# Optimization experiments

Hardware: AMD Instinct MI355X
Metric: run time of the kernel (lower is better)

## Reference

```python
import jax, jax.numpy as jnp
import numpy as np

IN_DIM = 256
LATENT = 1024
OUT_DIM = 256
B = 128
T = 1024


def setup_inputs() -> dict:
    key = jax.random.key(0)
    k1, k2, k3, k4 = jax.random.split(key, 4)
    # torch Linear weight layout: [out_features, in_features]
    bound_lin = 1.0 / np.sqrt(IN_DIM + LATENT)
    bound_dec = 1.0 / np.sqrt(LATENT)
    return {
        "x": jax.random.normal(k1, (B, T, IN_DIM), dtype=jnp.float32),
        "W_lin": jax.random.uniform(k2, (LATENT, IN_DIM + LATENT), minval=-bound_lin, maxval=bound_lin, dtype=jnp.float32),
        "W_dec": jax.random.uniform(k3, (OUT_DIM, LATENT), minval=-bound_dec, maxval=bound_dec, dtype=jnp.float32),
        "b_dec": jax.random.uniform(k4, (OUT_DIM,), minval=-bound_dec, maxval=bound_dec, dtype=jnp.float32),
    }


def reference(x, W_lin, W_dec, b_dec):
    # cat((x_t, h), dim=1) @ W_lin.T == x_t @ Wx.T + h @ Wh.T
    Wx = W_lin[:, :IN_DIM]      # [latent, in_dim]
    Wh = W_lin[:, IN_DIM:]      # [latent, latent]
    h0 = jnp.zeros((x.shape[0], LATENT), dtype=x.dtype)

    def step(h, x_t):
        h_new = jnp.tanh(x_t @ Wx.T + h @ Wh.T)
        return h_new, None

    # scan over time: x -> [T, B, in_dim]
    h_final, _ = jax.lax.scan(step, h0, jnp.swapaxes(x, 0, 1))
    return jnp.tanh(h_final @ W_dec.T + b_dec)
```

## Files before the change

### kernel.cpp

```cpp
#include <hip/hip_runtime.h>
#include <hip/hip_bf16.h>
#include <stdint.h>

#define B_    128
#define T_    1024
#define IN_   256
#define L_    1024
#define OUT_  256
#define KTOT  1280

#define GROUPS 8
#define WPG    32
#define NB     16
#define NC     32
#define PAD_K  1288
#define LDS_W_BYTES (NC * PAD_K * 2)
#define RED_BYTES   (8 * 4 * 64 * 4)
#define STILE_BYTES (16 * 32 * 2)
#define LDS_TOTAL   (LDS_W_BYTES + RED_BYTES + STILE_BYTES)

using short8 = __attribute__((ext_vector_type(8))) short;
using bf16x8 = __attribute__((ext_vector_type(8))) __bf16;
using f32x4  = __attribute__((ext_vector_type(4))) float;

__device__ __forceinline__ unsigned short f2b(float f) {
  unsigned u = __builtin_bit_cast(unsigned, f);
  u += 0x7FFFu + ((u >> 16) & 1u);
  return (unsigned short)(u >> 16);
}
__device__ __forceinline__ float b2f(unsigned short h) {
  unsigned u = ((unsigned)h) << 16;
  return __builtin_bit_cast(float, u);
}
__device__ __forceinline__ float fast_tanh(float z) {
  z = fminf(fmaxf(z, -30.f), 30.f);
  float e2 = __expf(2.f * z);
  return __fdividef(e2 - 1.f, e2 + 1.f);
}

__global__ __launch_bounds__(256, 1)
void rnn_persistent(const float* __restrict__ x, const float* __restrict__ Wlin,
                    unsigned short* __restrict__ h0buf, unsigned short* __restrict__ h1buf,
                    unsigned int* __restrict__ flags)
{
  extern __shared__ char smem[];
  short* Wlds = (short*)smem;
  float* red  = (float*)(smem + LDS_W_BYTES);
  unsigned short* stile = (unsigned short*)(smem + LDS_W_BYTES + RED_BYTES);

  const int tid = threadIdx.x;
  const int g   = blockIdx.x & 7;
  const int w   = blockIdx.x >> 3;
  const int bb  = g * NB;
  const int cc  = w * NC;
  unsigned int* myflag = flags + (size_t)(g * WPG + w) * 16;

  for (int r = 0; r < NC; ++r) {
    const float* wrow = Wlin + (size_t)(cc + r) * KTOT;
    for (int k = tid; k < KTOT; k += 256)
      Wlds[r * PAD_K + k] = (short)f2b(wrow[k]);
  }
  __syncthreads();

  const int wv   = tid >> 6;
  const int l    = tid & 63;
  const int lrow = l & 15;
  const int lk   = (l >> 4) * 8;

  for (int t = 0; t < T_; ++t) {
    const unsigned short* hcur = (t & 1) ? h1buf : h0buf;
    unsigned short*       hnxt = (t & 1) ? h0buf : h1buf;

    f32x4 acc0 = {0.f, 0.f, 0.f, 0.f};
    f32x4 acc1 = {0.f, 0.f, 0.f, 0.f};

    #pragma unroll
    for (int j = 0; j < 2; ++j) {
      const int kk    = wv + 4 * j;
      const int kbase = kk * 32 + lk;
      const float* xp = x + ((size_t)(bb + lrow) * T_ + t) * IN_ + kbase;
      f32x4 x0 = *(const f32x4*)xp;
      f32x4 x1 = *(const f32x4*)(xp + 4);
      short8 a;
      a[0] = (short)f2b(x0[0]); a[1] = (short)f2b(x0[1]);
      a[2] = (short)f2b(x0[2]); a[3] = (short)f2b(x0[3]);
      a[4] = (short)f2b(x1[0]); a[5] = (short)f2b(x1[1]);
      a[6] = (short)f2b(x1[2]); a[7] = (short)f2b(x1[3]);
      short8 b0 = *(const short8*)&Wlds[lrow        * PAD_K + kbase];
      short8 b1 = *(const short8*)&Wlds[(lrow + 16) * PAD_K + kbase];
      acc0 = __builtin_amdgcn_mfma_f32_16x16x32_bf16(
               __builtin_bit_cast(bf16x8, a), __builtin_bit_cast(bf16x8, b0), acc0, 0, 0, 0);
      acc1 = __builtin_amdgcn_mfma_f32_16x16x32_bf16(
               __builtin_bit_cast(bf16x8, a), __builtin_bit_cast(bf16x8, b1), acc1, 0, 0, 0);
    }

    if (t > 0) {
      if (wv == 0) {
        unsigned int* fp = flags + (size_t)(g * WPG + (l & 31)) * 16;
        while (true) {
          unsigned int v = __hip_atomic_load(fp, __ATOMIC_RELAXED, __HIP_MEMORY_SCOPE_AGENT);
          if (__all((int)(v >= (unsigned)t))) break;
          __builtin_amdgcn_s_sleep(1);
        }
      }
      __syncthreads();

      short8 hf[8];
      #pragma unroll
      for (int j = 2; j < 10; ++j) {
        const int kk    = wv + 4 * j;
        const int kbase = kk * 32 + lk - IN_;
        const unsigned short* p = hcur + (size_t)(bb + lrow) * L_ + kbase;
        asm volatile("global_load_dwordx4 %0, %1, off sc0 sc1"
                     : "=v"(hf[j - 2]) : "v"(p) : "memory");
      }
      asm volatile("s_waitcnt vmcnt(0)" ::: "memory");
      __builtin_amdgcn_sched_barrier(0);

      #pragma unroll
      for (int j = 2; j < 10; ++j) {
        const int kbase = (wv + 4 * j) * 32 + lk;
        short8 b0 = *(const short8*)&Wlds[lrow        * PAD_K + kbase];
        short8 b1 = *(const short8*)&Wlds[(lrow + 16) * PAD_K + kbase];
        acc0 = __builtin_amdgcn_mfma_f32_16x16x32_bf16(
                 __builtin_bit_cast(bf16x8, hf[j - 2]), __builtin_bit_cast(bf16x8, b0), acc0, 0, 0, 0);
        acc1 = __builtin_amdgcn_mfma_f32_16x16x32_bf16(
                 __builtin_bit_cast(bf16x8, hf[j - 2]), __builtin_bit_cast(bf16x8, b1), acc1, 0, 0, 0);
      }
    }

    #pragma unroll
    for (int j = 0; j < 4; ++j) {
      red[((wv * 2 + 0) * 4 + j) * 64 + l] = acc0[j];
      red[((wv * 2 + 1) * 4 + j) * 64 + l] = acc1[j];
    }
    __syncthreads();
    if (wv < 2) {
      const int tile = wv;
      #pragma unroll
      for (int j = 0; j < 4; ++j) {
        float s = red[((0 * 2 + tile) * 4 + j) * 64 + l]
                + red[((1 * 2 + tile) * 4 + j) * 64 + l]
                + red[((2 * 2 + tile) * 4 + j) * 64 + l]
                + red[((3 * 2 + tile) * 4 + j) * 64 + l];
        float hv = fast_tanh(s);
        const int row = (l >> 4) * 4 + j;
        const int col = tile * 16 + (l & 15);
        stile[row * 32 + col] = f2b(hv);
      }
    }
    __syncthreads();

    {
      const int row  = tid >> 4;
      const int dcol = tid & 15;
      unsigned int v = ((const unsigned int*)stile)[tid];
      unsigned int* dp = (unsigned int*)(hnxt + (size_t)(bb + row) * L_ + cc) + dcol;
      asm volatile("global_store_dword %0, %1, off sc0 sc1" :: "v"(dp), "v"(v) : "memory");
    }
    asm volatile("s_waitcnt vmcnt(0)" ::: "memory");
    __syncthreads();
    if (tid == 0)
      __hip_atomic_store(myflag, (unsigned)(t + 1), __ATOMIC_RELAXED, __HIP_MEMORY_SCOPE_AGENT);
  }
}

__global__ __launch_bounds__(256)
void decode_kernel(const unsigned short* __restrict__ hfin,
                   const float* __restrict__ Wdec, const float* __restrict__ bdec,
                   float* __restrict__ out)
{
  __shared__ float hrow[L_];
  const int b = blockIdx.x, tid = threadIdx.x;
  for (int k = tid; k < L_; k += 256)
    hrow[k] = b2f(hfin[b * L_ + k]);
  __syncthreads();
  float s = bdec[tid];
  const float* wr = Wdec + (size_t)tid * L_;
  #pragma unroll 4
  for (int k = 0; k < L_; k += 4) {
    f32x4 wq = *(const f32x4*)(wr + k);
    s += hrow[k] * wq[0] + hrow[k+1] * wq[1] + hrow[k+2] * wq[2] + hrow[k+3] * wq[3];
  }
  out[b * OUT_ + tid] = fast_tanh(s);
}

extern "C" void kernel_launch(void* const* d_in, const int* in_sizes, int n_in,
                              void* d_out, int out_size, void* d_ws, size_t ws_size,
                              hipStream_t stream)
{
  const float* x    = (const float*)d_in[0];
  const float* Wlin = (const float*)d_in[1];
  const float* Wdec = (const float*)d_in[2];
  const float* bdec = (const float*)d_in[3];
  float* out = (float*)d_out;

  unsigned short* h0 = (unsigned short*)d_ws;
  unsigned short* h1 = h0 + (size_t)B_ * L_;
  unsigned int* flags = (unsigned int*)((char*)d_ws + (size_t)2 * B_ * L_ * 2);

  hipMemsetAsync(flags, 0, (size_t)GROUPS * WPG * 16 * sizeof(unsigned int), stream);

  hipFuncSetAttribute((const void*)rnn_persistent,
                      hipFuncAttributeMaxDynamicSharedMemorySize, LDS_TOTAL);

  hipLaunchKernelGGL(rnn_persistent, dim3(GROUPS * WPG), dim3(256), LDS_TOTAL, stream,
                     x, Wlin, h0, h1, flags);
  hipLaunchKernelGGL(decode_kernel, dim3(B_), dim3(256), 0, stream,
                     h0, Wdec, bdec, out);
}
```

Measured before the change: 3.290 ms.

## Replace per-step flag barrier with sentinel-tagged 4-slot hidden-state ring

Drops the per-block progress flags and the spin on them. Hidden states now go into a 4-slot ring whose entries are reset to a NaN sentinel two steps ahead. Readers load h directly and reload any chunk still holding the sentinel, so data arrival itself acts as the sync and one __syncthreads plus the flag store are removed each step. A retry cap stops the spin after a fixed count and then goes ahead with possibly stale data, and correctness depends on store ordering across slots.

```diff
diff --git a/kernel.cpp b/kernel.cpp
--- a/kernel.cpp
+++ b/kernel.cpp
@@ -19,9 +19,14 @@
 #define STILE_BYTES (16 * 32 * 2)
 #define LDS_TOTAL   (LDS_W_BYTES + RED_BYTES + STILE_BYTES)
 
+#define SENT      0x7F807F80u
+#define SLOT      (B_ * L_)
+#define RETRY_CAP 20000
+
 using short8 = __attribute__((ext_vector_type(8))) short;
 using bf16x8 = __attribute__((ext_vector_type(8))) __bf16;
 using f32x4  = __attribute__((ext_vector_type(4))) float;
+using u32x4  = __attribute__((ext_vector_type(4))) unsigned;
 
 __device__ __forceinline__ unsigned short f2b(float f) {
   unsigned u = __builtin_bit_cast(unsigned, f);
@@ -37,11 +42,26 @@
   float e2 = __expf(2.f * z);
   return __fdividef(e2 - 1.f, e2 + 1.f);
 }
+__device__ __forceinline__ int chunk_ok(short8 c) {
+  u32x4 u = __builtin_bit_cast(u32x4, c);
+  return (u[0] != SENT) & (u[1] != SENT) & (u[2] != SENT) & (u[3] != SENT);
+}
+__device__ __forceinline__ void st_dw(unsigned int* p, unsigned int v) {
+  asm volatile("global_store_dword %0, %1, off sc0 sc1" :: "v"(p), "v"(v) : "memory");
+}
+__device__ __forceinline__ void ld_x4(short8& d, const unsigned short* p) {
+  asm volatile("global_load_dwordx4 %0, %1, off sc0 sc1" : "=v"(d) : "v"(p) : "memory");
+}
+
+__global__ void init_ws(unsigned int* ring_dw) {
+  size_t i = (size_t)blockIdx.x * 256 + threadIdx.x;
+  const size_t total = (size_t)4 * SLOT / 2;
+  for (size_t k = i; k < total; k += (size_t)256 * 256) ring_dw[k] = SENT;
+}
 
 __global__ __launch_bounds__(256, 1)
 void rnn_persistent(const float* __restrict__ x, const float* __restrict__ Wlin,
-                    unsigned short* __restrict__ h0buf, unsigned short* __restrict__ h1buf,
-                    unsigned int* __restrict__ flags)
+                    unsigned short* __restrict__ ring)
 {
   extern __shared__ char smem[];
   short* Wlds = (short*)smem;
@@ -53,7 +73,6 @@
   const int w   = blockIdx.x >> 3;
   const int bb  = g * NB;
   const int cc  = w * NC;
-  unsigned int* myflag = flags + (size_t)(g * WPG + w) * 16;
 
   for (int r = 0; r < NC; ++r) {
     const float* wrow = Wlin + (size_t)(cc + r) * KTOT;
@@ -66,10 +85,26 @@
   const int l    = tid & 63;
   const int lrow = l & 15;
   const int lk   = (l >> 4) * 8;
+  const int prow = tid >> 4;
+  const int pcol = tid & 15;
 
   for (int t = 0; t < T_; ++t) {
-    const unsigned short* hcur = (t & 1) ? h1buf : h0buf;
-    unsigned short*       hnxt = (t & 1) ? h0buf : h1buf;
+    unsigned short* hcur = ring + (size_t)(t & 3) * SLOT;
+    unsigned short* hnxt = ring + (size_t)((t + 1) & 3) * SLOT;
+
+    {
+      unsigned int* rp = (unsigned int*)(ring + (size_t)((t + 2) & 3) * SLOT
+                                         + (size_t)(bb + prow) * L_ + cc) + pcol;
+      st_dw(rp, SENT);
+    }
+
+    short8 hf[8];
+    const unsigned short* hbase = hcur + (size_t)(bb + lrow) * L_ + wv * 32 + lk;
+    if (t > 0) {
+      #pragma unroll
+      for (int j = 0; j < 8; ++j)
+        ld_x4(hf[j], hbase + j * 128);
+    }
 
     f32x4 acc0 = {0.f, 0.f, 0.f, 0.f};
     f32x4 acc1 = {0.f, 0.f, 0.f, 0.f};
@@ -95,37 +130,33 @@
     }
 
     if (t > 0) {
-      if (wv == 0) {
-        unsigned int* fp = flags + (size_t)(g * WPG + (l & 31)) * 16;
-        while (true) {
-          unsigned int v = __hip_atomic_load(fp, __ATOMIC_RELAXED, __HIP_MEMORY_SCOPE_AGENT);
-          if (__all((int)(v >= (unsigned)t))) break;
-          __builtin_amdgcn_s_sleep(1);
-        }
-      }
-      __syncthreads();
-
-      short8 hf[8];
-      #pragma unroll
-      for (int j = 2; j < 10; ++j) {
-        const int kk    = wv + 4 * j;
-        const int kbase = kk * 32 + lk - IN_;
-        const unsigned short* p = hcur + (size_t)(bb + lrow) * L_ + kbase;
-        asm volatile("global_load_dwordx4 %0, %1, off sc0 sc1"
-                     : "=v"(hf[j - 2]) : "v"(p) : "memory");
-      }
       asm volatile("s_waitcnt vmcnt(0)" ::: "memory");
       __builtin_amdgcn_sched_barrier(0);
 
+      bool okj[8] = {false, false, false, false, false, false, false, false};
+      int remaining = 8, tries = 0;
+      while (true) {
+        #pragma unroll
+        for (int j = 0; j < 8; ++j)
+          if (!okj[j] && __all(chunk_ok(hf[j]))) { okj[j] = true; --remaining; }
+        if (remaining == 0) break;
+        if (++tries > RETRY_CAP) break;
+        #pragma unroll
+        for (int j = 0; j < 8; ++j)
+          if (!okj[j]) ld_x4(hf[j], hbase + j * 128);
+        asm volatile("s_waitcnt vmcnt(0)" ::: "memory");
+        __builtin_amdgcn_sched_barrier(0);
+      }
+
       #pragma unroll
-      for (int j = 2; j < 10; ++j) {
-        const int kbase = (wv + 4 * j) * 32 + lk;
+      for (int j = 0; j < 8; ++j) {
+        const int kbase = IN_ + wv * 32 + j * 128 + lk;
         short8 b0 = *(const short8*)&Wlds[lrow        * PAD_K + kbase];
         short8 b1 = *(const short8*)&Wlds[(lrow + 16) * PAD_K + kbase];
         acc0 = __builtin_amdgcn_mfma_f32_16x16x32_bf16(
-                 __builtin_bit_cast(bf16x8, hf[j - 2]), __builtin_bit_cast(bf16x8, b0), acc0, 0, 0, 0);
+                 __builtin_bit_cast(bf16x8, hf[j]), __builtin_bit_cast(bf16x8, b0), acc0, 0, 0, 0);
         acc1 = __builtin_amdgcn_mfma_f32_16x16x32_bf16(
-                 __builtin_bit_cast(bf16x8, hf[j - 2]), __builtin_bit_cast(bf16x8, b1), acc1, 0, 0, 0);
+                 __builtin_bit_cast(bf16x8, hf[j]), __builtin_bit_cast(bf16x8, b1), acc1, 0, 0, 0);
       }
     }
 
@@ -144,24 +175,17 @@
                 + red[((2 * 2 + tile) * 4 + j) * 64 + l]
                 + red[((3 * 2 + tile) * 4 + j) * 64 + l];
         float hv = fast_tanh(s);
-        const int row = (l >> 4) * 4 + j;
-        const int col = tile * 16 + (l & 15);
-        stile[row * 32 + col] = f2b(hv);
+        stile[((l >> 4) * 4 + j) * 32 + tile * 16 + (l & 15)] = f2b(hv);
       }
     }
     __syncthreads();
 
+    asm volatile("s_waitcnt vmcnt(0)" ::: "memory");
     {
-      const int row  = tid >> 4;
-      const int dcol = tid & 15;
       unsigned int v = ((const unsigned int*)stile)[tid];
-      unsigned int* dp = (unsigned int*)(hnxt + (size_t)(bb + row) * L_ + cc) + dcol;
-      asm volatile("global_store_dword %0, %1, off sc0 sc1" :: "v"(dp), "v"(v) : "memory");
-    }
-    asm volatile("s_waitcnt vmcnt(0)" ::: "memory");
-    __syncthreads();
-    if (tid == 0)
-      __hip_atomic_store(myflag, (unsigned)(t + 1), __ATOMIC_RELAXED, __HIP_MEMORY_SCOPE_AGENT);
+      unsigned int* dp = (unsigned int*)(hnxt + (size_t)(bb + prow) * L_ + cc) + pcol;
+      st_dw(dp, v);
+    }
   }
 }
 
@@ -195,17 +219,15 @@
   const float* bdec = (const float*)d_in[3];
   float* out = (float*)d_out;
 
-  unsigned short* h0 = (unsigned short*)d_ws;
-  unsigned short* h1 = h0 + (size_t)B_ * L_;
-  unsigned int* flags = (unsigned int*)((char*)d_ws + (size_t)2 * B_ * L_ * 2);
-
-  hipMemsetAsync(flags, 0, (size_t)GROUPS * WPG * 16 * sizeof(unsigned int), stream);
+  unsigned short* ring = (unsigned short*)d_ws;
 
   hipFuncSetAttribute((const void*)rnn_persistent,
                       hipFuncAttributeMaxDynamicSharedMemorySize, LDS_TOTAL);
 
+  hipLaunchKernelGGL(init_ws, dim3(256), dim3(256), 0, stream,
+                     (unsigned int*)ring);
   hipLaunchKernelGGL(rnn_persistent, dim3(GROUPS * WPG), dim3(256), LDS_TOTAL, stream,
-                     x, Wlin, h0, h1, flags);
+                     x, Wlin, ring);
   hipLaunchKernelGGL(decode_kernel, dim3(B_), dim3(256), 0, stream,
-                     h0, Wdec, bdec, out);
-}
+                     ring, Wdec, bdec, out);
+}
```

Measured after the change: 4.521 ms. 37.4% more time.

## Halve workgroups per batch group and consume hidden-state slices as producers signal

Applied to the files above, without the earlier changes.

The partition changes from 32 to 16 workgroups per batch group, so each workgroup computes 64 latent columns. The input-projection weights now live in registers, and LDS holds only the recurrent weights. The global barrier, where one wave waited on all 32 flags, is replaced by per-wave polling of just the 4 producer flags that wave depends on. Each wave then loads and multiplies hidden-state slices as soon as they are ready, so compute overlaps with waiting and a block-wide sync goes away. The output staging tile is dropped in favour of direct 16-bit stores. This trades half as many CUs doing twice the MFMA work per step for fewer flags to poll and finer-grained overlap.

```diff
diff --git a/kernel.cpp b/kernel.cpp
--- a/kernel.cpp
+++ b/kernel.cpp
@@ -10,14 +10,13 @@
 #define KTOT  1280
 
 #define GROUPS 8
-#define WPG    32
+#define WPG    16
 #define NB     16
-#define NC     32
-#define PAD_K  1288
-#define LDS_W_BYTES (NC * PAD_K * 2)
-#define RED_BYTES   (8 * 4 * 64 * 4)
-#define STILE_BYTES (16 * 32 * 2)
-#define LDS_TOTAL   (LDS_W_BYTES + RED_BYTES + STILE_BYTES)
+#define NC     64
+#define PADW   1032
+#define LDS_W_BYTES (NC * PADW * 2)
+#define RED_BYTES   (4 * 4 * 4 * 64 * 4)
+#define LDS_TOTAL   (LDS_W_BYTES + RED_BYTES)
 
 using short8 = __attribute__((ext_vector_type(8))) short;
 using bf16x8 = __attribute__((ext_vector_type(8))) __bf16;
@@ -36,6 +35,20 @@
   z = fminf(fmaxf(z, -30.f), 30.f);
   float e2 = __expf(2.f * z);
   return __fdividef(e2 - 1.f, e2 + 1.f);
+}
+__device__ __forceinline__ void st_us(unsigned short* p, unsigned short v) {
+  asm volatile("global_store_short %0, %1, off sc0 sc1" :: "v"(p), "v"(v) : "memory");
+}
+__device__ __forceinline__ void ld_x4(short8& d, const unsigned short* p) {
+  asm volatile("global_load_dwordx4 %0, %1, off sc0 sc1" : "=v"(d) : "v"(p) : "memory");
+}
+__device__ __forceinline__ short8 cvt8(f32x4 a, f32x4 b) {
+  short8 v;
+  v[0] = (short)f2b(a[0]); v[1] = (short)f2b(a[1]);
+  v[2] = (short)f2b(a[2]); v[3] = (short)f2b(a[3]);
+  v[4] = (short)f2b(b[0]); v[5] = (short)f2b(b[1]);
+  v[6] = (short)f2b(b[2]); v[7] = (short)f2b(b[3]);
+  return v;
 }
 
 __global__ __launch_bounds__(256, 1)
@@ -46,118 +59,112 @@
   extern __shared__ char smem[];
   short* Wlds = (short*)smem;
   float* red  = (float*)(smem + LDS_W_BYTES);
-  unsigned short* stile = (unsigned short*)(smem + LDS_W_BYTES + RED_BYTES);
 
   const int tid = threadIdx.x;
   const int g   = blockIdx.x & 7;
   const int w   = blockIdx.x >> 3;
   const int bb  = g * NB;
   const int cc  = w * NC;
+
+  for (int r = 0; r < NC; ++r) {
+    const float* wrow = Wlin + (size_t)(cc + r) * KTOT + IN_;
+    for (int k = tid; k < L_; k += 256)
+      Wlds[r * PADW + k] = (short)f2b(wrow[k]);
+  }
+
+  const int wv  = tid >> 6;
+  const int l   = tid & 63;
+  const int lr  = l & 15;
+  const int lk8 = (l >> 4) * 8;
+
+  short8 wx[4][2];
+  #pragma unroll
+  for (int nt = 0; nt < 4; ++nt) {
+    #pragma unroll
+    for (int ks = 0; ks < 2; ++ks) {
+      const float* wp = Wlin + (size_t)(cc + nt * 16 + lr) * KTOT + wv * 64 + ks * 32 + lk8;
+      wx[nt][ks] = cvt8(*(const f32x4*)wp, *(const f32x4*)(wp + 4));
+    }
+  }
+  __syncthreads();
+
   unsigned int* myflag = flags + (size_t)(g * WPG + w) * 16;
-
-  for (int r = 0; r < NC; ++r) {
-    const float* wrow = Wlin + (size_t)(cc + r) * KTOT;
-    for (int k = tid; k < KTOT; k += 256)
-      Wlds[r * PAD_K + k] = (short)f2b(wrow[k]);
-  }
-  __syncthreads();
-
-  const int wv   = tid >> 6;
-  const int l    = tid & 63;
-  const int lrow = l & 15;
-  const int lk   = (l >> 4) * 8;
 
   for (int t = 0; t < T_; ++t) {
     const unsigned short* hcur = (t & 1) ? h1buf : h0buf;
     unsigned short*       hnxt = (t & 1) ? h0buf : h1buf;
 
-    f32x4 acc0 = {0.f, 0.f, 0.f, 0.f};
-    f32x4 acc1 = {0.f, 0.f, 0.f, 0.f};
-
-    #pragma unroll
-    for (int j = 0; j < 2; ++j) {
-      const int kk    = wv + 4 * j;
-      const int kbase = kk * 32 + lk;
-      const float* xp = x + ((size_t)(bb + lrow) * T_ + t) * IN_ + kbase;
-      f32x4 x0 = *(const f32x4*)xp;
-      f32x4 x1 = *(const f32x4*)(xp + 4);
-      short8 a;
-      a[0] = (short)f2b(x0[0]); a[1] = (short)f2b(x0[1]);
-      a[2] = (short)f2b(x0[2]); a[3] = (short)f2b(x0[3]);
-      a[4] = (short)f2b(x1[0]); a[5] = (short)f2b(x1[1]);
-      a[6] = (short)f2b(x1[2]); a[7] = (short)f2b(x1[3]);
-      short8 b0 = *(const short8*)&Wlds[lrow        * PAD_K + kbase];
-      short8 b1 = *(const short8*)&Wlds[(lrow + 16) * PAD_K + kbase];
-      acc0 = __builtin_amdgcn_mfma_f32_16x16x32_bf16(
-               __builtin_bit_cast(bf16x8, a), __builtin_bit_cast(bf16x8, b0), acc0, 0, 0, 0);
-      acc1 = __builtin_amdgcn_mfma_f32_16x16x32_bf16(
-               __builtin_bit_cast(bf16x8, a), __builtin_bit_cast(bf16x8, b1), acc1, 0, 0, 0);
+    f32x4 acc[4] = {{0,0,0,0},{0,0,0,0},{0,0,0,0},{0,0,0,0}};
+
+    #pragma unroll
+    for (int ks = 0; ks < 2; ++ks) {
+      const float* xp = x + ((size_t)(bb + lr) * T_ + t) * IN_ + wv * 64 + ks * 32 + lk8;
+      short8 a = cvt8(*(const f32x4*)xp, *(const f32x4*)(xp + 4));
+      #pragma unroll
+      for (int nt = 0; nt < 4; ++nt)
+        acc[nt] = __builtin_amdgcn_mfma_f32_16x16x32_bf16(
+                    __builtin_bit_cast(bf16x8, a), __builtin_bit_cast(bf16x8, wx[nt][ks]),
+                    acc[nt], 0, 0, 0);
     }
 
     if (t > 0) {
-      if (wv == 0) {
-        unsigned int* fp = flags + (size_t)(g * WPG + (l & 31)) * 16;
-        while (true) {
-          unsigned int v = __hip_atomic_load(fp, __ATOMIC_RELAXED, __HIP_MEMORY_SCOPE_AGENT);
-          if (__all((int)(v >= (unsigned)t))) break;
+      const unsigned short* hrow = hcur + (size_t)(bb + lr) * L_;
+      short8 hb[4][2];
+      unsigned pending = 0xFu;
+      while (pending) {
+        unsigned fv = 0;
+        if (l < 4)
+          fv = __hip_atomic_load(flags + (size_t)(g * WPG + 4 * wv + l) * 16,
+                                 __ATOMIC_RELAXED, __HIP_MEMORY_SCOPE_AGENT);
+        unsigned avail = (unsigned)__ballot(l < 4 && fv >= (unsigned)t) & pending;
+        if (avail) {
+          #pragma unroll
+          for (int p = 0; p < 4; ++p)
+            if (avail & (1u << p)) {
+              ld_x4(hb[p][0], hrow + (4 * wv + p) * 64 + lk8);
+              ld_x4(hb[p][1], hrow + (4 * wv + p) * 64 + 32 + lk8);
+            }
+          asm volatile("s_waitcnt vmcnt(0)" ::: "memory");
+          __builtin_amdgcn_sched_barrier(0);
+          #pragma unroll
+          for (int p = 0; p < 4; ++p)
+            if (avail & (1u << p)) {
+              #pragma unroll
+              for (int ks = 0; ks < 2; ++ks) {
+                const int kb = (4 * wv + p) * 64 + ks * 32 + lk8;
+                #pragma unroll
+                for (int nt = 0; nt < 4; ++nt) {
+                  short8 bf = *(const short8*)&Wlds[(nt * 16 + lr) * PADW + kb];
+                  acc[nt] = __builtin_amdgcn_mfma_f32_16x16x32_bf16(
+                              __builtin_bit_cast(bf16x8, hb[p][ks]),
+                              __builtin_bit_cast(bf16x8, bf), acc[nt], 0, 0, 0);
+                }
+              }
+            }
+          pending &= ~avail;
+        } else {
           __builtin_amdgcn_s_sleep(1);
         }
       }
-      __syncthreads();
-
-      short8 hf[8];
+    }
+
+    #pragma unroll
+    for (int nt = 0; nt < 4; ++nt)
       #pragma unroll
-      for (int j = 2; j < 10; ++j) {
-        const int kk    = wv + 4 * j;
-        const int kbase = kk * 32 + lk - IN_;
-        const unsigned short* p = hcur + (size_t)(bb + lrow) * L_ + kbase;
-        asm volatile("global_load_dwordx4 %0, %1, off sc0 sc1"
-                     : "=v"(hf[j - 2]) : "v"(p) : "memory");
-      }
-      asm volatile("s_waitcnt vmcnt(0)" ::: "memory");
-      __builtin_amdgcn_sched_barrier(0);
-
-      #pragma unroll
-      for (int j = 2; j < 10; ++j) {
-        const int kbase = (wv + 4 * j) * 32 + lk;
-        short8 b0 = *(const short8*)&Wlds[lrow        * PAD_K + kbase];
-        short8 b1 = *(const short8*)&Wlds[(lrow + 16) * PAD_K + kbase];
-        acc0 = __builtin_amdgcn_mfma_f32_16x16x32_bf16(
-                 __builtin_bit_cast(bf16x8, hf[j - 2]), __builtin_bit_cast(bf16x8, b0), acc0, 0, 0, 0);
-        acc1 = __builtin_amdgcn_mfma_f32_16x16x32_bf16(
-                 __builtin_bit_cast(bf16x8, hf[j - 2]), __builtin_bit_cast(bf16x8, b1), acc1, 0, 0, 0);
-      }
-    }
+      for (int j = 0; j < 4; ++j)
+        red[((wv * 4 + nt) * 4 + j) * 64 + l] = acc[nt][j];
+    __syncthreads();
 
     #pragma unroll
     for (int j = 0; j < 4; ++j) {
-      red[((wv * 2 + 0) * 4 + j) * 64 + l] = acc0[j];
-      red[((wv * 2 + 1) * 4 + j) * 64 + l] = acc1[j];
-    }
-    __syncthreads();
-    if (wv < 2) {
-      const int tile = wv;
-      #pragma unroll
-      for (int j = 0; j < 4; ++j) {
-        float s = red[((0 * 2 + tile) * 4 + j) * 64 + l]
-                + red[((1 * 2 + tile) * 4 + j) * 64 + l]
-                + red[((2 * 2 + tile) * 4 + j) * 64 + l]
-                + red[((3 * 2 + tile) * 4 + j) * 64 + l];
-        float hv = fast_tanh(s);
-        const int row = (l >> 4) * 4 + j;
-        const int col = tile * 16 + (l & 15);
-        stile[row * 32 + col] = f2b(hv);
-      }
-    }
-    __syncthreads();
-
-    {
-      const int row  = tid >> 4;
-      const int dcol = tid & 15;
-      unsigned int v = ((const unsigned int*)stile)[tid];
-      unsigned int* dp = (unsigned int*)(hnxt + (size_t)(bb + row) * L_ + cc) + dcol;
-      asm volatile("global_store_dword %0, %1, off sc0 sc1" :: "v"(dp), "v"(v) : "memory");
-    }
+      float s = red[((0 * 4 + wv) * 4 + j) * 64 + l]
+              + red[((1 * 4 + wv) * 4 + j) * 64 + l]
+              + red[((2 * 4 + wv) * 4 + j) * 64 + l]
+              + red[((3 * 4 + wv) * 4 + j) * 64 + l];
+      float hv = fast_tanh(s);
+      st_us(hnxt + (size_t)(bb + (l >> 4) * 4 + j) * L_ + cc + wv * 16 + lr, f2b(hv));
+    }
+
     asm volatile("s_waitcnt vmcnt(0)" ::: "memory");
     __syncthreads();
     if (tid == 0)
```

Result: slower. 4.127 ms (+25.5%).
